# Kernel optimization log

Measured on AMD Instinct MI355X. Metric: run time of the kernel, lower is better.

## Reference

```python
import jax, jax.numpy as jnp
import numpy as np

K = 20
EPS = 1e-5
SLOPE = 0.2


def knn_idx(x, k):
    # x: (B, C, N) -> (B, N, k) indices of k nearest neighbors (incl. self)
    xx = jnp.sum(x * x, axis=1)  # (B, N)
    # negative squared distance: largest = nearest
    pd = 2.0 * jnp.einsum('bcn,bcm->bnm', x, x) - xx[:, :, None] - xx[:, None, :]
    return jax.lax.top_k(pd, k)[1]


def graph_feature(x, k):
    # x: (B, C, N) -> (B, 2C, N, k) edge features [x_j - x_i, x_i]
    idx = knn_idx(x, k)                       # (B, N, k)
    xt = jnp.transpose(x, (0, 2, 1))          # (B, N, C)
    feat = jax.vmap(lambda xb, ib: xb[ib])(xt, idx)  # (B, N, k, C)
    center = xt[:, :, None, :]
    out = jnp.concatenate([feat - center, jnp.broadcast_to(center, feat.shape)], axis=-1)
    return jnp.transpose(out, (0, 3, 1, 2))   # (B, 2C, N, k)


def conv_bn_lrelu2d(x, W, g, b):
    # 1x1 Conv2d (no bias) + BatchNorm2d (batch stats, train mode) + LeakyReLU(0.2)
    y = jnp.einsum('oc,bcnk->bonk', W, x)
    m = jnp.mean(y, axis=(0, 2, 3), keepdims=True)
    v = jnp.var(y, axis=(0, 2, 3), keepdims=True)
    y = (y - m) * jax.lax.rsqrt(v + EPS) * g[None, :, None, None] + b[None, :, None, None]
    return jnp.where(y > 0, y, SLOPE * y)


def conv_bn_lrelu1d(x, W, g, b):
    y = jnp.einsum('oc,bcn->bon', W, x)
    m = jnp.mean(y, axis=(0, 2), keepdims=True)
    v = jnp.var(y, axis=(0, 2), keepdims=True)
    y = (y - m) * jax.lax.rsqrt(v + EPS) * g[None, :, None] + b[None, :, None]
    return jnp.where(y > 0, y, SLOPE * y)


def setup_inputs() -> dict:
    key = jax.random.key(0)
    ks = jax.random.split(key, 8)
    B, N, C = 8, 2048, 3
    emb = 1024
    fix = 1  # output == 'pointwise'
    xyz = jax.random.normal(ks[0], (B, N, C), dtype=jnp.float32)
    def w(k, o, i):
        return jax.random.normal(k, (o, i), dtype=jnp.float32) * (1.0 / np.sqrt(i))
    inp = {
        'xyz': xyz,
        'W1': w(ks[1], 64, 2 * C), 'g1': jnp.ones((64,), jnp.float32), 'b1': jnp.zeros((64,), jnp.float32),
        'W2': w(ks[2], 64, 128), 'g2': jnp.ones((64,), jnp.float32), 'b2': jnp.zeros((64,), jnp.float32),
        'W3': w(ks[3], 128, 128), 'g3': jnp.ones((128,), jnp.float32), 'b3': jnp.zeros((128,), jnp.float32),
        'W4': w(ks[4], 256 + fix, 256), 'g4': jnp.ones((256 + fix,), jnp.float32), 'b4': jnp.zeros((256 + fix,), jnp.float32),
        'W5': w(ks[5], emb, 512 + fix), 'g5': jnp.ones((emb,), jnp.float32), 'b5': jnp.zeros((emb,), jnp.float32),
    }
    return inp


def reference(xyz, W1, g1, b1, W2, g2, b2, W3, g3, b3, W4, g4, b4, W5, g5, b5):
    x0 = jnp.transpose(xyz, (0, 2, 1))  # (B, 3, N)
    B, _, N = x0.shape

    x = graph_feature(x0, K)            # (B, 6, N, k)
    x1 = jnp.max(conv_bn_lrelu2d(x, W1, g1, b1), axis=-1)   # (B, 64, N)

    x = graph_feature(x1, K)            # (B, 128, N, k)
    x2 = jnp.max(conv_bn_lrelu2d(x, W2, g2, b2), axis=-1)   # (B, 64, N)

    x = graph_feature(x2, K)            # (B, 128, N, k)
    x3 = jnp.max(conv_bn_lrelu2d(x, W3, g3, b3), axis=-1)   # (B, 128, N)

    x = graph_feature(x3, K)            # (B, 256, N, k)
    x4 = jnp.max(conv_bn_lrelu2d(x, W4, g4, b4), axis=-1)   # (B, 257, N)

    x_f = jnp.concatenate([x1, x2, x3, x4], axis=1)          # (B, 513, N)
    _x = conv_bn_lrelu1d(x_f, W5, g5, b5)                    # (B, emb, N)

    gmax = jnp.max(_x, axis=-1)   # (B, emb)
    gavg = jnp.mean(_x, axis=-1)  # (B, emb)
    g = jnp.concatenate([gmax, gavg], axis=1)[:, :, None]    # (B, 2*emb, 1)
    g = jnp.broadcast_to(g, (B, g.shape[1], N))
    return jnp.concatenate([g, x0, x_f], axis=1)             # (B, 2*emb+3+513, N)
```

## Files before the change

### kernel.cpp

```cpp
#include <hip/hip_runtime.h>
#include <math.h>

#define BB 8
#define NN 2048
#define KK 20
#define OCH 2564
#define OCN ((size_t)OCH*NN)
#define EPSD 1e-5
#define SLOPED 0.2
#define TS 64

#define WS_PD   ((size_t)0)
#define WS_YMX  ((size_t)4194304)
#define WS_YMN  ((size_t)8404992)
#define WS_XA   ((size_t)12615680)
#define WS_XB   ((size_t)14712832)
#define WS_U    ((size_t)16809984)
#define WS_V    ((size_t)21020672)
#define WS_IDX  ((size_t)25231360)
#define WS_XX   ((size_t)25559040)
#define WS_WTF  ((size_t)25575424)
#define WS_WTD  ((size_t)25608448)
#define WS_W5T  ((size_t)25641472)
#define WS_Y5   ((size_t)0)
#define WS_S1   ((size_t)26166784)
#define WS_S2   (WS_S1 + 2048)
#define WS_SC   (WS_S2 + 2048)
#define WS_SH   (WS_SC + 2048)

static inline int cdiv(int a, int b){ return (a+b-1)/b; }

__global__ void k_prep_x0(const float* __restrict__ xyz, float* __restrict__ out,
                          float* __restrict__ xA){
  int id = blockIdx.x*256 + threadIdx.x;
  if (id >= BB*NN) return;
  int b = id / NN, n = id % NN;
  const float* p = xyz + ((size_t)b*NN + n)*3;
  float* o = out + (size_t)b*OCN + (size_t)2048*NN + n;
  o[0] = p[0]; o[(size_t)NN] = p[1]; o[2*(size_t)NN] = p[2];
  float* xa = xA + (size_t)b*3*NN + n;
  xa[0] = p[0]; xa[(size_t)NN] = p[1]; xa[2*(size_t)NN] = p[2];
}

__global__ void k_xx32(const float* __restrict__ x, int C, float* __restrict__ xx){
  int b = blockIdx.y;
  int n = blockIdx.x*256 + threadIdx.x;
  const float* p = x + (size_t)b*C*NN + n;
  float a;
  if (C <= 8){
    a = 0.f;
    for (int c = 0; c < C; c++){ float v = p[(size_t)c*NN]; float s = v*v; a = a + s; }
  } else {
    float r0,r1,r2,r3,r4,r5,r6,r7;
    { float v;
      v = p[0];            r0 = v*v;
      v = p[(size_t)1*NN]; r1 = v*v;
      v = p[(size_t)2*NN]; r2 = v*v;
      v = p[(size_t)3*NN]; r3 = v*v;
      v = p[(size_t)4*NN]; r4 = v*v;
      v = p[(size_t)5*NN]; r5 = v*v;
      v = p[(size_t)6*NN]; r6 = v*v;
      v = p[(size_t)7*NN]; r7 = v*v;
    }
    for (int i = 8; i < C; i += 8){
      float v;
      v = p[(size_t)(i+0)*NN]; r0 = r0 + v*v;
      v = p[(size_t)(i+1)*NN]; r1 = r1 + v*v;
      v = p[(size_t)(i+2)*NN]; r2 = r2 + v*v;
      v = p[(size_t)(i+3)*NN]; r3 = r3 + v*v;
      v = p[(size_t)(i+4)*NN]; r4 = r4 + v*v;
      v = p[(size_t)(i+5)*NN]; r5 = r5 + v*v;
      v = p[(size_t)(i+6)*NN]; r6 = r6 + v*v;
      v = p[(size_t)(i+7)*NN]; r7 = r7 + v*v;
    }
    a = ((r0+r1)+(r2+r3)) + ((r4+r5)+(r6+r7));
  }
  xx[b*NN + n] = a;
}

__global__ __launch_bounds__(256) void k_pd4(const float* __restrict__ x, int C, int b0,
                     const float* __restrict__ xx, float* __restrict__ wsbase,
                     unsigned long long o0, unsigned long long o1,
                     unsigned long long o2, unsigned long long o3){
  int z = blockIdx.z;
  unsigned long long off = (z==0)?o0:((z==1)?o1:((z==2)?o2:o3));
  float* pd = wsbase + off;
  int b = b0 + z;
  __shared__ float As[8][128];
  __shared__ float Bs[8][128];
  int n0 = blockIdx.y*128, m0 = blockIdx.x*128;
  int tid = threadIdx.x;
  int ty = tid / 16, tx = tid % 16;
  const float* xb = x + (size_t)b*C*NN;
  float acc[8][8] = {};
  for (int c0 = 0; c0 < C; c0 += 8){
    #pragma unroll
    for (int rr = 0; rr < 4; rr++){
      int t2 = tid + rr*256;
      int c = t2 >> 7, col = t2 & 127;
      int cc = c0 + c;
      float av = 0.f, bv = 0.f;
      if (cc < C){ av = xb[(size_t)cc*NN + n0 + col]; bv = xb[(size_t)cc*NN + m0 + col]; }
      As[c][col] = av; Bs[c][col] = bv;
    }
    __syncthreads();
    #pragma unroll
    for (int c = 0; c < 8; c++){
      float4 a0 = *reinterpret_cast<const float4*>(&As[c][ty*8]);
      float4 a1 = *reinterpret_cast<const float4*>(&As[c][ty*8+4]);
      float4 b0v = *reinterpret_cast<const float4*>(&Bs[c][tx*4]);
      float4 b1v = *reinterpret_cast<const float4*>(&Bs[c][64 + tx*4]);
      float a[8]  = {a0.x,a0.y,a0.z,a0.w,a1.x,a1.y,a1.z,a1.w};
      float bv[8] = {b0v.x,b0v.y,b0v.z,b0v.w,b1v.x,b1v.y,b1v.z,b1v.w};
      #pragma unroll
      for (int i=0;i<8;i++)
        #pragma unroll
        for (int j=0;j<8;j++)
          acc[i][j] = fmaf(a[i], bv[j], acc[i][j]);
    }
    __syncthreads();
  }
  const float* xxb = xx + b*NN;
  float xm0[4], xm1[4];
  #pragma unroll
  for (int j=0;j<4;j++){ xm0[j] = xxb[m0 + tx*4 + j]; xm1[j] = xxb[m0 + 64 + tx*4 + j]; }
  #pragma unroll
  for (int i=0;i<8;i++){
    int n = n0 + ty*8 + i;
    float xn = xxb[n];
    float4 v0, v1;
    v0.x = (2.f*acc[i][0] - xn) - xm0[0];
    v0.y = (2.f*acc[i][1] - xn) - xm0[1];
    v0.z = (2.f*acc[i][2] - xn) - xm0[2];
    v0.w = (2.f*acc[i][3] - xn) - xm0[3];
    v1.x = (2.f*acc[i][4] - xn) - xm1[0];
    v1.y = (2.f*acc[i][5] - xn) - xm1[1];
    v1.z = (2.f*acc[i][6] - xn) - xm1[2];
    v1.w = (2.f*acc[i][7] - xn) - xm1[3];
    *reinterpret_cast<float4*>(&pd[(size_t)n*NN + m0 + tx*4])      = v0;
    *reinterpret_cast<float4*>(&pd[(size_t)n*NN + m0 + 64 + tx*4]) = v1;
  }
}

__global__ __launch_bounds__(256) void k_topk4(const float* __restrict__ wsbase,
                     unsigned long long o0, unsigned long long o1,
                     unsigned long long o2, unsigned long long o3,
                     int b0, int* __restrict__ idx){
  int z = blockIdx.y;
  unsigned long long off = (z==0)?o0:((z==1)?o1:((z==2)?o2:o3));
  const float* pdb = wsbase + off;
  int b = b0 + z;
  int lane = threadIdx.x & 63;
  int w = threadIdx.x >> 6;
  int n = blockIdx.x*4 + w;
  const float* row = pdb + (size_t)n*NN;
  float vals[KK]; int inds[KK];
  #pragma unroll
  for (int i=0;i<KK;i++){ vals[i] = -INFINITY; inds[i] = NN; }
  for (int c = 0; c < NN/64; c++){
    int m = c*64 + lane;
    float v = row[m];
    if (v > vals[KK-1]){
      #pragma unroll
      for (int i=KK-1;i>0;--i){
        if (vals[i-1] < v){ vals[i]=vals[i-1]; inds[i]=inds[i-1]; }
      }
      bool done = false;
      #pragma unroll
      for (int i=0;i<KK;i++){
        bool pl = (!done) && (vals[i] < v);
        if (pl){ vals[i]=v; inds[i]=m; done=true; }
      }
    }
  }
  int* op = idx + ((size_t)b*NN + n)*KK;
  #pragma unroll 1
  for (int r = 0; r < KK; r++){
    float bv = vals[0]; int bi = inds[0];
    #pragma unroll
    for (int s = 1; s < 64; s <<= 1){
      float ov = __shfl_xor(bv, s);
      int   oi = __shfl_xor(bi, s);
      if (ov > bv || (ov == bv && oi < bi)){ bv = ov; bi = oi; }
    }
    if (inds[0] == bi){
      #pragma unroll
      for (int i=0;i<KK-1;i++){ vals[i]=vals[i+1]; inds[i]=inds[i+1]; }
      vals[KK-1] = -INFINITY; inds[KK-1] = NN;
    }
    if (lane == 0) op[r] = bi;
  }
}

__global__ void k_wt(const float* __restrict__ W, float* __restrict__ wtf,
                     float* __restrict__ wtd, int Cin, int O,
                     double* __restrict__ s1, double* __restrict__ s2){
  if (blockIdx.x == 0){
    int t = threadIdx.x;
    #pragma unroll
    for (int i=0;i<4;i++){ s1[t*4+i] = 0.0; s2[t*4+i] = 0.0; }
  }
  int id = blockIdx.x*256 + threadIdx.x;
  if (id >= Cin*O) return;
  int c = id / O, o = id % O;
  float wf = W[(size_t)o*(2*Cin) + c];
  float wc = W[(size_t)o*(2*Cin) + Cin + c];
  wtf[(size_t)c*O + o] = wf;
  wtd[(size_t)c*O + o] = wc - wf;
}

__global__ void k_wt5(const float* __restrict__ W5, float* __restrict__ w5t){
  int id = blockIdx.x*256 + threadIdx.x;
  if (id >= 513*1024) return;
  int c = id / 1024, o = id % 1024;
  w5t[(size_t)c*1024 + o] = W5[(size_t)o*513 + c];
}

__global__ __launch_bounds__(256) void k_gemm_uv(
    const float* __restrict__ x, int C, int O,
    const float* __restrict__ wtf, const float* __restrict__ wtd,
    float* __restrict__ u, float* __restrict__ v){
  __shared__ float Xs[8][TS];
  __shared__ float Wfs[8][TS];
  __shared__ float Wds[8][TS];
  int b = blockIdx.z;
  int n0 = blockIdx.y*TS, o0 = blockIdx.x*TS;
  int tid = threadIdx.x, tx = tid%16, ty = tid/16;
  const float* xb = x + (size_t)b*C*NN;
  double au[4][4] = {};
  double av[4][4] = {};
  for (int c0 = 0; c0 < C; c0 += 8){
    int r = tid/64, col = tid%64;
    #pragma unroll
    for (int rr=0;rr<2;rr++){
      int c = c0 + r + rr*4;
      float xv=0.f, wfv=0.f, wdv=0.f;
      if (c < C){
        xv = xb[(size_t)c*NN + n0 + col];
        if (o0+col < O){
          wfv = wtf[(size_t)c*O + o0+col];
          wdv = wtd[(size_t)c*O + o0+col];
        }
      }
      Xs[r+rr*4][col]=xv; Wfs[r+rr*4][col]=wfv; Wds[r+rr*4][col]=wdv;
    }
    __syncthreads();
    #pragma unroll
    for (int c=0;c<8;c++){
      double a[4], f[4], d[4];
      #pragma unroll
      for (int i=0;i<4;i++) a[i] = (double)Xs[c][ty*4+i];
      #pragma unroll
      for (int j=0;j<4;j++) f[j] = (double)Wfs[c][tx*4+j];
      #pragma unroll
      for (int j=0;j<4;j++) d[j] = (double)Wds[c][tx*4+j];
      #pragma unroll
      for (int i=0;i<4;i++)
        #pragma unroll
        for (int j=0;j<4;j++){
          au[i][j] = fma(a[i], f[j], au[i][j]);
          av[i][j] = fma(a[i], d[j], av[i][j]);
        }
    }
    __syncthreads();
  }
  #pragma unroll
  for (int i=0;i<4;i++){
    int n = n0 + ty*4 + i;
    #pragma unroll
    for (int j=0;j<4;j++){
      int o = o0 + tx*4 + j;
      if (o < O){
        u[((size_t)b*NN + n)*O + o] = (float)au[i][j];
        v[((size_t)b*NN + n)*O + o] = (float)av[i][j];
      }
    }
  }
}

#define NT 32
__global__ __launch_bounds__(256) void k_passB(
  const float* __restrict__ u, const float* __restrict__ v, const int* __restrict__ idx,
  int O, int OT, float* __restrict__ ymax, float* __restrict__ ymin,
  double* __restrict__ s1, double* __restrict__ s2){
  __shared__ int ids[NT*KK];
  int b = blockIdx.y, n0 = blockIdx.x*NT;
  int tid = threadIdx.x;
  for (int t = tid; t < NT*KK; t += 256) ids[t] = idx[((size_t)b*NN + n0)*KK + t];
  __syncthreads();
  int nsplit = 256/OT;
  int ob = tid % OT, ns = tid / OT;
  int nper = NT / nsplit;
  const float* ub = u + (size_t)b*NN*O;
  const float* vb = v + (size_t)b*NN*O;
  for (int o = ob; o < O; o += 256){
    double s1p = 0.0, s2p = 0.0;
    for (int ni = ns*nper; ni < (ns+1)*nper; ni++){
      double su=0.0, sq=0.0;
      float mx=-INFINITY, mn=INFINITY;
      #pragma unroll
      for (int k=0;k<KK;k++){
        int j = ids[ni*KK + k];
        float uu = ub[(size_t)j*O + o];
        double ud = (double)uu;
        su += ud; sq += ud*ud;
        mx = fmaxf(mx, uu); mn = fminf(mn, uu);
      }
      float vv = vb[(size_t)(n0+ni)*O + o];
      double vd = (double)vv;
      s1p += su + (double)KK*vd;
      s2p += sq + 2.0*vd*su + (double)KK*vd*vd;
      size_t yo = ((size_t)b*NN + n0 + ni)*O + o;
      ymax[yo] = mx + vv; ymin[yo] = mn + vv;
    }
    atomicAdd(&s1[o], s1p);
    atomicAdd(&s2[o], s2p);
  }
}

__global__ void k_stats_fin(const double* __restrict__ s1, const double* __restrict__ s2,
                            const float* __restrict__ g, const float* __restrict__ bb,
                            int O, double M, double* __restrict__ scale, double* __restrict__ shift){
  int o = blockIdx.x*256 + threadIdx.x;
  if (o >= O) return;
  double mean = s1[o]/M;
  double var  = s2[o]/M - mean*mean;
  double sc = (double)g[o] / sqrt(var + EPSD);
  scale[o] = sc;
  shift[o] = (double)bb[o] - mean*sc;
}

__global__ __launch_bounds__(256) void k_passD(const float* __restrict__ ymax,
  const float* __restrict__ ymin, const double* __restrict__ scale,
  const double* __restrict__ shift, int O, float* __restrict__ xout,
  float* __restrict__ xnext){
  __shared__ float t[64][65];
  int b = blockIdx.z, n0 = blockIdx.y*64, o0 = blockIdx.x*64;
  int tid = threadIdx.x;
  int col = tid % 64, rr = tid / 64;
  int o = o0 + col;
  bool ov = (o < O);
  double sc = ov ? scale[o] : 0.0;
  double sh = ov ? shift[o] : 0.0;
  const float* src = (sc >= 0.0) ? ymax : ymin;
  for (int p = 0; p < 16; p++){
    int n = n0 + p*4 + rr;
    float y = ov ? src[((size_t)b*NN + n)*O + o] : 0.f;
    double z = sc*(double)y + sh;
    z = z > 0.0 ? z : SLOPED*z;
    t[p*4+rr][col] = (float)z;
  }
  __syncthreads();
  float* xb = xout + (size_t)b*OCN;
  for (int p = 0; p < 16; p++){
    int row = p*4 + rr;
    if (o0 + row < O){
      float val = t[col][row];
      xb[(size_t)(o0+row)*NN + n0 + col] = val;
      if (xnext) xnext[((size_t)b*O + o0+row)*NN + n0 + col] = val;
    }
  }
}

__global__ __launch_bounds__(256) void k_conv5g(const float* __restrict__ xf,
                                                const float* __restrict__ w5t,
                                                float* __restrict__ y5){
  __shared__ float Wsh[8][128];
  __shared__ float Xs[8][128];
  int o0 = blockIdx.x*128, n0 = blockIdx.y*128, b = blockIdx.z;
  int tid = threadIdx.x;
  int ty = tid / 16, tx = tid % 16;
  const float* xb = xf + (size_t)b*OCN;
  float acc[8][8] = {};
  for (int c0 = 0; c0 < 513; c0 += 8){
    #pragma unroll
    for (int rr = 0; rr < 4; rr++){
      int t2 = tid + rr*256;
      int c = t2 >> 7, col = t2 & 127;
      int cc = c0 + c;
      float wv = 0.f, xv = 0.f;
      if (cc < 513){
        wv = w5t[(size_t)cc*1024 + o0 + col];
        xv = xb[(size_t)cc*NN + n0 + col];
      }
      Wsh[c][col] = wv; Xs[c][col] = xv;
    }
    __syncthreads();
    #pragma unroll
    for (int c = 0; c < 8; c++){
      float4 w0 = *reinterpret_cast<const float4*>(&Wsh[c][ty*8]);
      float4 w1 = *reinterpret_cast<const float4*>(&Wsh[c][ty*8+4]);
      float4 x0 = *reinterpret_cast<const float4*>(&Xs[c][tx*4]);
      float4 x1 = *reinterpret_cast<const float4*>(&Xs[c][64 + tx*4]);
      float wr[8] = {w0.x,w0.y,w0.z,w0.w,w1.x,w1.y,w1.z,w1.w};
      float xr[8] = {x0.x,x0.y,x0.z,x0.w,x1.x,x1.y,x1.z,x1.w};
      #pragma unroll
      for (int i=0;i<8;i++)
        #pragma unroll
        for (int j=0;j<8;j++)
          acc[i][j] = fmaf(wr[i], xr[j], acc[i][j]);
    }
    __syncthreads();
  }
  #pragma unroll
  for (int i=0;i<8;i++){
    int o = o0 + ty*8 + i;
    float* yr = y5 + ((size_t)b*1024 + o)*NN;
    float4 v0 = {acc[i][0], acc[i][1], acc[i][2], acc[i][3]};
    float4 v1 = {acc[i][4], acc[i][5], acc[i][6], acc[i][7]};
    *reinterpret_cast<float4*>(&yr[n0 + tx*4])      = v0;
    *reinterpret_cast<float4*>(&yr[n0 + 64 + tx*4]) = v1;
  }
}

__global__ __launch_bounds__(256) void k_stats5_v2(const float* __restrict__ y5,
                                                   const float* __restrict__ g,
                                                   const float* __restrict__ bb,
                                                   double* __restrict__ scale,
                                                   double* __restrict__ shift){
  int o = blockIdx.x;
  __shared__ double sh1[256], sh2[256];
  double a = 0.0, q = 0.0;
  for (int bn = threadIdx.x; bn < BB*NN; bn += 256){
    int b = bn >> 11, n = bn & 2047;
    double yv = (double)y5[((size_t)b*1024 + o)*NN + n];
    a += yv; q += yv*yv;
  }
  sh1[threadIdx.x] = a; sh2[threadIdx.x] = q;
  __syncthreads();
  for (int s = 128; s > 0; s >>= 1){
    if (threadIdx.x < s){ sh1[threadIdx.x] += sh1[threadIdx.x+s]; sh2[threadIdx.x] += sh2[threadIdx.x+s]; }
    __syncthreads();
  }
  if (threadIdx.x == 0){
    double M = (double)(BB*NN);
    double mean = sh1[0]/M;
    double var  = sh2[0]/M - mean*mean;
    double sc = (double)g[o]/sqrt(var + EPSD);
    scale[o] = sc;
    shift[o] = (double)bb[o] - mean*sc;
  }
}

__global__ __launch_bounds__(256) void k_final5_v2(const float* __restrict__ y5,
                                                   const double* __restrict__ scale,
                                                   const double* __restrict__ shift,
                                                   float* __restrict__ out){
  int o = blockIdx.x, b = blockIdx.y;
  __shared__ double smx[256], ssm[256];
  double sc = scale[o], sh = shift[o];
  double mx = -INFINITY, sm = 0.0;
  const float* yrow = y5 + ((size_t)b*1024 + o)*NN;
  for (int n = threadIdx.x; n < NN; n += 256){
    double z = sc*(double)yrow[n] + sh;
    z = z > 0.0 ? z : SLOPED*z;
    mx = fmax(mx, z); sm += z;
  }
  smx[threadIdx.x] = mx; ssm[threadIdx.x] = sm;
  __syncthreads();
  for (int s = 128; s > 0; s >>= 1){
    if (threadIdx.x < s){
      smx[threadIdx.x] = fmax(smx[threadIdx.x], smx[threadIdx.x+s]);
      ssm[threadIdx.x] += ssm[threadIdx.x+s];
    }
    __syncthreads();
  }
  float vg = (float)smx[0];
  float va = (float)(ssm[0]*(1.0/NN));
  float* ob = out + (size_t)b*OCN;
  for (int n = threadIdx.x; n < NN; n += 256){
    ob[(size_t)o*NN + n] = vg;
    ob[(size_t)(1024+o)*NN + n] = va;
  }
}

extern "C" void kernel_launch(void* const* d_in, const int* in_sizes, int n_in,
                              void* d_out, int out_size, void* d_ws, size_t ws_size,
                              hipStream_t stream){
  const float* xyz = (const float*)d_in[0];
  float* out = (float*)d_out;
  float* ws  = (float*)d_ws;

  const float* Wp[5] = {(const float*)d_in[1],(const float*)d_in[4],(const float*)d_in[7],(const float*)d_in[10],(const float*)d_in[13]};
  const float* Gp[5] = {(const float*)d_in[2],(const float*)d_in[5],(const float*)d_in[8],(const float*)d_in[11],(const float*)d_in[14]};
  const float* Bp[5] = {(const float*)d_in[3],(const float*)d_in[6],(const float*)d_in[9],(const float*)d_in[12],(const float*)d_in[15]};
  int Cin[4]  = {3, 64, 64, 128};
  int Oc[4]   = {64, 64, 128, 257};
  int xoutc[4]= {2051, 2115, 2179, 2307};

  float* ymx  = ws + WS_YMX;
  float* ymn  = ws + WS_YMN;
  float* xA   = ws + WS_XA;
  float* xB   = ws + WS_XB;
  float* u    = ws + WS_U;
  float* v    = ws + WS_V;
  int*   idx  = (int*)(ws + WS_IDX);
  float* xx   = ws + WS_XX;
  float* wtf  = ws + WS_WTF;
  float* wtd  = ws + WS_WTD;
  float* w5t  = ws + WS_W5T;
  float* y5   = ws + WS_Y5;
  double* s1d = (double*)(ws + WS_S1);
  double* s2d = (double*)(ws + WS_S2);
  double* scd = (double*)(ws + WS_SC);
  double* shd = (double*)(ws + WS_SH);

  k_prep_x0<<<cdiv(BB*NN,256), 256, 0, stream>>>(xyz, out, xA);

  for (int t = 0; t < 4; t++){
    int C = Cin[t], O = Oc[t];
    const float* xin = (t % 2 == 0) ? xA : xB;
    float* xnext = (t == 3) ? nullptr : ((t % 2 == 0) ? xB : xA);
    k_wt  <<<cdiv(C*O,256), 256, 0, stream>>>(Wp[t], wtf, wtd, C, O, s1d, s2d);
    k_xx32<<<dim3(NN/256, BB), 256, 0, stream>>>(xin, C, xx);
    int OT = (O <= 64) ? 64 : ((O <= 128) ? 128 : 256);
    for (int bg = 0; bg < 2; bg++){
      k_pd4  <<<dim3(NN/128, NN/128, 4), 256, 0, stream>>>(xin, C, bg*4, xx, ws,
               (unsigned long long)WS_PD, (unsigned long long)WS_YMX,
               (unsigned long long)WS_YMN, (unsigned long long)WS_U);
      k_topk4<<<dim3(NN/4, 4), 256, 0, stream>>>(ws,
               (unsigned long long)WS_PD, (unsigned long long)WS_YMX,
               (unsigned long long)WS_YMN, (unsigned long long)WS_U,
               bg*4, idx);
    }
    k_gemm_uv<<<dim3(cdiv(O,TS), NN/TS, BB), 256, 0, stream>>>(xin, C, O, wtf, wtd, u, v);
    k_passB  <<<dim3(NN/NT, BB), 256, 0, stream>>>(u, v, idx, O, OT, ymx, ymn, s1d, s2d);
    k_stats_fin<<<cdiv(O,256), 256, 0, stream>>>(s1d, s2d, Gp[t], Bp[t], O, (double)((size_t)BB*NN*KK), scd, shd);
    k_passD<<<dim3(cdiv(O,TS), NN/TS, BB), 256, 0, stream>>>(ymx, ymn, scd, shd, O, out + (size_t)xoutc[t]*NN, xnext);
  }

  k_wt5   <<<cdiv(513*1024,256), 256, 0, stream>>>(Wp[4], w5t);
  k_conv5g<<<dim3(1024/128, NN/128, BB), 256, 0, stream>>>(out + (size_t)2051*NN, w5t, y5);
  k_stats5_v2<<<1024, 256, 0, stream>>>(y5, Gp[4], Bp[4], scd, shd);
  k_final5_v2<<<dim3(1024, BB), 256, 0, stream>>>(y5, scd, shd, out);
}
```

Baseline: 2.438 ms.

## Merge weight-transpose kernels, fold stats finalize into passD, read layer inputs from output

All per-layer weight transposes and the W5 transpose move into one kernel launched up front, and the BN accumulator zeroing moves into k_xx32. Stat finalization is folded into k_passD, which now computes scale and shift per block in shared memory. The ping-pong xA/xB scratch copies are removed: later layers read their input directly from the output tensor with a batch stride, which drops a duplicate write per layer. This cuts launches and memory traffic, but inputs are now read with a larger batch stride and passD recomputes stats redundantly per block.

```diff
diff --git a/kernel.cpp b/kernel.cpp
--- a/kernel.cpp
+++ b/kernel.cpp
@@ -13,39 +13,65 @@
 #define WS_PD   ((size_t)0)
 #define WS_YMX  ((size_t)4194304)
 #define WS_YMN  ((size_t)8404992)
-#define WS_XA   ((size_t)12615680)
-#define WS_XB   ((size_t)14712832)
-#define WS_U    ((size_t)16809984)
-#define WS_V    ((size_t)21020672)
-#define WS_IDX  ((size_t)25231360)
-#define WS_XX   ((size_t)25559040)
-#define WS_WTF  ((size_t)25575424)
-#define WS_WTD  ((size_t)25608448)
-#define WS_W5T  ((size_t)25641472)
+#define WS_U    ((size_t)12615680)
+#define WS_V    ((size_t)16826368)
+#define WS_IDX  ((size_t)21037056)
+#define WS_XX   ((size_t)21364736)
+#define WS_WTF  ((size_t)21381120)
+#define WS_WTD  ((size_t)21426496)
+#define WS_W5T  ((size_t)21471872)
 #define WS_Y5   ((size_t)0)
-#define WS_S1   ((size_t)26166784)
+#define WS_S1   ((size_t)21997184)
 #define WS_S2   (WS_S1 + 2048)
 #define WS_SC   (WS_S2 + 2048)
 #define WS_SH   (WS_SC + 2048)
 
 static inline int cdiv(int a, int b){ return (a+b-1)/b; }
 
-__global__ void k_prep_x0(const float* __restrict__ xyz, float* __restrict__ out,
-                          float* __restrict__ xA){
+__global__ void k_prep_x0(const float* __restrict__ xyz, float* __restrict__ out){
   int id = blockIdx.x*256 + threadIdx.x;
   if (id >= BB*NN) return;
   int b = id / NN, n = id % NN;
   const float* p = xyz + ((size_t)b*NN + n)*3;
   float* o = out + (size_t)b*OCN + (size_t)2048*NN + n;
   o[0] = p[0]; o[(size_t)NN] = p[1]; o[2*(size_t)NN] = p[2];
-  float* xa = xA + (size_t)b*3*NN + n;
-  xa[0] = p[0]; xa[(size_t)NN] = p[1]; xa[2*(size_t)NN] = p[2];
-}
-
-__global__ void k_xx32(const float* __restrict__ x, int C, float* __restrict__ xx){
+}
+
+__global__ void k_wt_all(const float* __restrict__ W1, const float* __restrict__ W2,
+                         const float* __restrict__ W3, const float* __restrict__ W4,
+                         const float* __restrict__ W5,
+                         float* __restrict__ wtf, float* __restrict__ wtd,
+                         float* __restrict__ w5t){
+  int id = blockIdx.x*256 + threadIdx.x;
+  if (id < 513*1024){
+    int c = id / 1024, o = id % 1024;
+    w5t[(size_t)c*1024 + o] = W5[(size_t)o*513 + c];
+  }
+  if (id < 45376){
+    const float* W; int C, O; int base;
+    if (id < 192)        { W = W1; C = 3;   O = 64;  base = 0; }
+    else if (id < 4288)  { W = W2; C = 64;  O = 64;  base = 192; }
+    else if (id < 12480) { W = W3; C = 64;  O = 128; base = 4288; }
+    else                 { W = W4; C = 128; O = 257; base = 12480; }
+    int r = id - base;
+    int c = r / O, o = r % O;
+    float wf = W[(size_t)o*(2*C) + c];
+    float wc = W[(size_t)o*(2*C) + C + c];
+    wtf[base + (size_t)c*O + o] = wf;
+    wtd[base + (size_t)c*O + o] = wc - wf;
+  }
+}
+
+__global__ void k_xx32(const float* __restrict__ x, int C, size_t bs, float* __restrict__ xx,
+                       double* __restrict__ s1, double* __restrict__ s2){
+  if (blockIdx.x == 0 && blockIdx.y == 0){
+    int t = threadIdx.x;
+    #pragma unroll
+    for (int i=0;i<4;i++){ s1[t*4+i] = 0.0; s2[t*4+i] = 0.0; }
+  }
   int b = blockIdx.y;
   int n = blockIdx.x*256 + threadIdx.x;
-  const float* p = x + (size_t)b*C*NN + n;
+  const float* p = x + (size_t)b*bs + n;
   float a;
   if (C <= 8){
     a = 0.f;
@@ -78,7 +104,7 @@
   xx[b*NN + n] = a;
 }
 
-__global__ __launch_bounds__(256) void k_pd4(const float* __restrict__ x, int C, int b0,
+__global__ __launch_bounds__(256) void k_pd4(const float* __restrict__ x, int C, size_t bs, int b0,
                      const float* __restrict__ xx, float* __restrict__ wsbase,
                      unsigned long long o0, unsigned long long o1,
                      unsigned long long o2, unsigned long long o3){
@@ -91,7 +117,7 @@
   int n0 = blockIdx.y*128, m0 = blockIdx.x*128;
   int tid = threadIdx.x;
   int ty = tid / 16, tx = tid % 16;
-  const float* xb = x + (size_t)b*C*NN;
+  const float* xb = x + (size_t)b*bs;
   float acc[8][8] = {};
   for (int c0 = 0; c0 < C; c0 += 8){
     #pragma unroll
@@ -192,32 +218,8 @@
   }
 }
 
-__global__ void k_wt(const float* __restrict__ W, float* __restrict__ wtf,
-                     float* __restrict__ wtd, int Cin, int O,
-                     double* __restrict__ s1, double* __restrict__ s2){
-  if (blockIdx.x == 0){
-    int t = threadIdx.x;
-    #pragma unroll
-    for (int i=0;i<4;i++){ s1[t*4+i] = 0.0; s2[t*4+i] = 0.0; }
-  }
-  int id = blockIdx.x*256 + threadIdx.x;
-  if (id >= Cin*O) return;
-  int c = id / O, o = id % O;
-  float wf = W[(size_t)o*(2*Cin) + c];
-  float wc = W[(size_t)o*(2*Cin) + Cin + c];
-  wtf[(size_t)c*O + o] = wf;
-  wtd[(size_t)c*O + o] = wc - wf;
-}
-
-__global__ void k_wt5(const float* __restrict__ W5, float* __restrict__ w5t){
-  int id = blockIdx.x*256 + threadIdx.x;
-  if (id >= 513*1024) return;
-  int c = id / 1024, o = id % 1024;
-  w5t[(size_t)c*1024 + o] = W5[(size_t)o*513 + c];
-}
-
 __global__ __launch_bounds__(256) void k_gemm_uv(
-    const float* __restrict__ x, int C, int O,
+    const float* __restrict__ x, int C, int O, size_t bs,
     const float* __restrict__ wtf, const float* __restrict__ wtd,
     float* __restrict__ u, float* __restrict__ v){
   __shared__ float Xs[8][TS];
@@ -226,7 +228,7 @@
   int b = blockIdx.z;
   int n0 = blockIdx.y*TS, o0 = blockIdx.x*TS;
   int tid = threadIdx.x, tx = tid%16, ty = tid/16;
-  const float* xb = x + (size_t)b*C*NN;
+  const float* xb = x + (size_t)b*bs;
   double au[4][4] = {};
   double av[4][4] = {};
   for (int c0 = 0; c0 < C; c0 += 8){
@@ -318,30 +320,31 @@
   }
 }
 
-__global__ void k_stats_fin(const double* __restrict__ s1, const double* __restrict__ s2,
-                            const float* __restrict__ g, const float* __restrict__ bb,
-                            int O, double M, double* __restrict__ scale, double* __restrict__ shift){
-  int o = blockIdx.x*256 + threadIdx.x;
-  if (o >= O) return;
-  double mean = s1[o]/M;
-  double var  = s2[o]/M - mean*mean;
-  double sc = (double)g[o] / sqrt(var + EPSD);
-  scale[o] = sc;
-  shift[o] = (double)bb[o] - mean*sc;
-}
-
 __global__ __launch_bounds__(256) void k_passD(const float* __restrict__ ymax,
-  const float* __restrict__ ymin, const double* __restrict__ scale,
-  const double* __restrict__ shift, int O, float* __restrict__ xout,
-  float* __restrict__ xnext){
+  const float* __restrict__ ymin, const double* __restrict__ s1,
+  const double* __restrict__ s2, const float* __restrict__ g,
+  const float* __restrict__ bb, int O, double M, float* __restrict__ xout){
   __shared__ float t[64][65];
+  __shared__ double s_sc[64], s_sh[64];
   int b = blockIdx.z, n0 = blockIdx.y*64, o0 = blockIdx.x*64;
   int tid = threadIdx.x;
+  if (tid < 64){
+    int o = o0 + tid;
+    double sc = 0.0, sh = 0.0;
+    if (o < O){
+      double mean = s1[o]/M;
+      double var  = s2[o]/M - mean*mean;
+      sc = (double)g[o] / sqrt(var + EPSD);
+      sh = (double)bb[o] - mean*sc;
+    }
+    s_sc[tid] = sc; s_sh[tid] = sh;
+  }
+  __syncthreads();
   int col = tid % 64, rr = tid / 64;
   int o = o0 + col;
   bool ov = (o < O);
-  double sc = ov ? scale[o] : 0.0;
-  double sh = ov ? shift[o] : 0.0;
+  double sc = s_sc[col];
+  double sh = s_sh[col];
   const float* src = (sc >= 0.0) ? ymax : ymin;
   for (int p = 0; p < 16; p++){
     int n = n0 + p*4 + rr;
@@ -354,11 +357,7 @@
   float* xb = xout + (size_t)b*OCN;
   for (int p = 0; p < 16; p++){
     int row = p*4 + rr;
-    if (o0 + row < O){
-      float val = t[col][row];
-      xb[(size_t)(o0+row)*NN + n0 + col] = val;
-      if (xnext) xnext[((size_t)b*O + o0+row)*NN + n0 + col] = val;
-    }
+    if (o0 + row < O) xb[(size_t)(o0+row)*NN + n0 + col] = t[col][row];
   }
 }
 
@@ -486,12 +485,12 @@
   const float* Bp[5] = {(const float*)d_in[3],(const float*)d_in[6],(const float*)d_in[9],(const float*)d_in[12],(const float*)d_in[15]};
   int Cin[4]  = {3, 64, 64, 128};
   int Oc[4]   = {64, 64, 128, 257};
+  int xinc[4] = {2048, 2051, 2115, 2179};
   int xoutc[4]= {2051, 2115, 2179, 2307};
+  int woff[4] = {0, 192, 4288, 12480};
 
   float* ymx  = ws + WS_YMX;
   float* ymn  = ws + WS_YMN;
-  float* xA   = ws + WS_XA;
-  float* xB   = ws + WS_XB;
   float* u    = ws + WS_U;
   float* v    = ws + WS_V;
   int*   idx  = (int*)(ws + WS_IDX);
@@ -505,17 +504,16 @@
   double* scd = (double*)(ws + WS_SC);
   double* shd = (double*)(ws + WS_SH);
 
-  k_prep_x0<<<cdiv(BB*NN,256), 256, 0, stream>>>(xyz, out, xA);
+  k_prep_x0<<<cdiv(BB*NN,256), 256, 0, stream>>>(xyz, out);
+  k_wt_all <<<cdiv(513*1024,256), 256, 0, stream>>>(Wp[0], Wp[1], Wp[2], Wp[3], Wp[4], wtf, wtd, w5t);
 
   for (int t = 0; t < 4; t++){
     int C = Cin[t], O = Oc[t];
-    const float* xin = (t % 2 == 0) ? xA : xB;
-    float* xnext = (t == 3) ? nullptr : ((t % 2 == 0) ? xB : xA);
-    k_wt  <<<cdiv(C*O,256), 256, 0, stream>>>(Wp[t], wtf, wtd, C, O, s1d, s2d);
-    k_xx32<<<dim3(NN/256, BB), 256, 0, stream>>>(xin, C, xx);
+    const float* xin = out + (size_t)xinc[t]*NN;
+    k_xx32<<<dim3(NN/256, BB), 256, 0, stream>>>(xin, C, OCN, xx, s1d, s2d);
     int OT = (O <= 64) ? 64 : ((O <= 128) ? 128 : 256);
     for (int bg = 0; bg < 2; bg++){
-      k_pd4  <<<dim3(NN/128, NN/128, 4), 256, 0, stream>>>(xin, C, bg*4, xx, ws,
+      k_pd4  <<<dim3(NN/128, NN/128, 4), 256, 0, stream>>>(xin, C, OCN, bg*4, xx, ws,
                (unsigned long long)WS_PD, (unsigned long long)WS_YMX,
                (unsigned long long)WS_YMN, (unsigned long long)WS_U);
       k_topk4<<<dim3(NN/4, 4), 256, 0, stream>>>(ws,
@@ -523,13 +521,12 @@
                (unsigned long long)WS_YMN, (unsigned long long)WS_U,
                bg*4, idx);
     }
-    k_gemm_uv<<<dim3(cdiv(O,TS), NN/TS, BB), 256, 0, stream>>>(xin, C, O, wtf, wtd, u, v);
+    k_gemm_uv<<<dim3(cdiv(O,TS), NN/TS, BB), 256, 0, stream>>>(xin, C, O, OCN, wtf + woff[t], wtd + woff[t], u, v);
     k_passB  <<<dim3(NN/NT, BB), 256, 0, stream>>>(u, v, idx, O, OT, ymx, ymn, s1d, s2d);
-    k_stats_fin<<<cdiv(O,256), 256, 0, stream>>>(s1d, s2d, Gp[t], Bp[t], O, (double)((size_t)BB*NN*KK), scd, shd);
-    k_passD<<<dim3(cdiv(O,TS), NN/TS, BB), 256, 0, stream>>>(ymx, ymn, scd, shd, O, out + (size_t)xoutc[t]*NN, xnext);
-  }
-
-  k_wt5   <<<cdiv(513*1024,256), 256, 0, stream>>>(Wp[4], w5t);
+    k_passD  <<<dim3(cdiv(O,TS), NN/TS, BB), 256, 0, stream>>>(ymx, ymn, s1d, s2d, Gp[t], Bp[t], O,
+               (double)((size_t)BB*NN*KK), out + (size_t)xoutc[t]*NN);
+  }
+
   k_conv5g<<<dim3(1024/128, NN/128, BB), 256, 0, stream>>>(out + (size_t)2051*NN, w5t, y5);
   k_stats5_v2<<<1024, 256, 0, stream>>>(y5, Gp[4], Bp[4], scd, shd);
   k_final5_v2<<<dim3(1024, BB), 256, 0, stream>>>(y5, scd, shd, out);
```

Result: no change. 2.422 ms, median of 2 (-0.6%).
